# Optimization experiments

Measured on AMD Instinct MI355X. Metric: run time of the kernel, lower is better.

The kernel has to match this reference:

```python
import jax, jax.numpy as jnp
import numpy as np

N_NODES = 100000
N_EDGES = 3200000
D = 32


def _gat(x, edge_index, W, att_s, att_d, bias, heads, ch, neg_slope):
    """PyG-style GATConv (shared lin for src/dst, add_self_loops=False).
    x: [N, D_in], edge_index: [2, E], W: [heads*ch, D_in],
    att_s/att_d: [heads, ch], bias: [heads*ch]. Returns [N, heads*ch]."""
    n = x.shape[0]
    h = (x @ W.T).reshape(n, heads, ch)                      # [N,H,C]
    a_s = (h * att_s[None]).sum(-1)                           # [N,H]
    a_d = (h * att_d[None]).sum(-1)                           # [N,H]
    src, dst = edge_index[0], edge_index[1]
    logits = jax.nn.leaky_relu(a_s[src] + a_d[dst], neg_slope)  # [E,H]
    # segment softmax over edges grouped by destination node
    m = jax.ops.segment_max(logits, dst, num_segments=n)     # [N,H]
    m = jnp.where(jnp.isfinite(m), m, 0.0)                    # nodes w/ no in-edges
    ex = jnp.exp(logits - m[dst])                             # [E,H]
    denom = jax.ops.segment_sum(ex, dst, num_segments=n)     # [N,H]
    alpha = ex / (denom[dst] + 1e-16)                         # [E,H]
    out = jax.ops.segment_sum(alpha[:, :, None] * h[src], dst, num_segments=n)  # [N,H,C]
    return out.reshape(n, heads * ch) + bias


def setup_inputs() -> dict:
    key = jax.random.key(0)
    ks = jax.random.split(key, 16)
    x = jax.random.normal(ks[0], (N_NODES, D), dtype=jnp.float32)
    edge_index = jax.random.randint(ks[1], (2, N_EDGES), 0, N_NODES, dtype=jnp.int64)
    s = 1.0 / np.sqrt(D)
    return {
        "x": x,
        "edge_index": edge_index,
        "W1": jax.random.normal(ks[2], (32, D), dtype=jnp.float32) * s,
        "att_s1": jax.random.normal(ks[3], (2, 16), dtype=jnp.float32) * 0.05,
        "att_d1": jax.random.normal(ks[4], (2, 16), dtype=jnp.float32) * 0.05,
        "b1": jnp.full((32,), 0.1, dtype=jnp.float32),
        "ea1": jnp.ones((1,), dtype=jnp.float32),  # edge_activator
        "W2": jax.random.normal(ks[5], (32, 32), dtype=jnp.float32) * s,
        "att_s2": jax.random.normal(ks[6], (2, 16), dtype=jnp.float32) * 0.05,
        "att_d2": jax.random.normal(ks[7], (2, 16), dtype=jnp.float32) * 0.05,
        "b2": jnp.full((32,), 0.1, dtype=jnp.float32),
        "W3": jax.random.normal(ks[8], (32, 32), dtype=jnp.float32) * s,
        "att_s3": jax.random.normal(ks[9], (1, 32), dtype=jnp.float32) * 0.05,
        "att_d3": jax.random.normal(ks[10], (1, 32), dtype=jnp.float32) * 0.05,
        "b3": jnp.full((32,), 0.1, dtype=jnp.float32),
    }


def reference(x, edge_index, W1, att_s1, att_d1, b1, ea1,
              W2, att_s2, att_d2, b2, W3, att_s3, att_d3, b3):
    # --- layer 1 (negative_slope=0.01) ---
    h = _gat(x, edge_index, W1, att_s1, att_d1, b1, heads=2, ch=16, neg_slope=0.01)
    scale = jnp.tanh(ea1)[0]
    scale = jnp.where(scale < 0.1, 1.0, scale)  # 'continue' branch skips the scaling
    h = h * scale
    h = h + 0.05 * jax.lax.stop_gradient(h)      # h + 0.05*h.detach()
    h = jax.nn.elu(h)                            # eval path (training=False)
    h = jnp.clip(h, -3.0, 3.0)
    # --- layer 2 (default negative_slope=0.2) ---
    h = _gat(h, edge_index, W2, att_s2, att_d2, b2, heads=2, ch=16, neg_slope=0.2)
    h = jax.nn.elu(h)
    h = jnp.clip(h, -3.0, 3.0)
    # --- layer 3: heads=1, concat=False ---
    out = _gat(h, edge_index, W3, att_s3, att_d3, b3, heads=1, ch=32, neg_slope=0.2)
    return out
```

## Files before the change

kernel.cpp:

```cpp
#include <hip/hip_runtime.h>
#include <hip/hip_bf16.h>
#include <hip/hip_fp16.h>


#define NPB  128
#define CAPB 6144
#define PAD_SENTINEL 0xFFFFFFFFu

template <int H, int NL>
__device__ __forceinline__ void transform_body(
    const float* __restrict__ in, const float* __restrict__ W,
    const float* __restrict__ att_s, const float* __restrict__ att_d,
    __half* __restrict__ h16, float* __restrict__ a_s, float* __restrict__ a_d,
    int node0, int nlim, float (*Wl)[33], float (*xs)[32]) {
    constexpr int C = 32 / H;
    constexpr int NTH = NL * 32;
    int t = threadIdx.x;
    for (int i = t; i < 1024; i += NTH) Wl[i >> 5][i & 31] = W[i];
    int nl = t >> 5, o = t & 31;
    int node = node0 + nl;
    xs[nl][o] = (node < nlim) ? in[(size_t)node * 32 + o] : 0.f;
    __syncthreads();
    float acc = 0.f;
#pragma unroll
    for (int k = 0; k < 32; k++) acc = fmaf(xs[nl][k], Wl[o][k], acc);
    if (node < nlim) {
        h16[(size_t)node * 32 + o] = __float2half_rn(acc);
        float vs = acc * att_s[o];
        float vd = acc * att_d[o];
#pragma unroll
        for (int m = C / 2; m >= 1; m >>= 1) {
            vs += __shfl_xor(vs, m, 64);
            vd += __shfl_xor(vd, m, 64);
        }
        if ((o % C) == 0) {
            int hh = o / C;
            a_s[node * H + hh] = vs;
            a_d[node * H + hh] = vd;
        }
    }
}

__global__ void __launch_bounds__(1024)
k_bin_t1(const int* __restrict__ src, const int* __restrict__ dst,
         int* __restrict__ bucket_cursor, unsigned int* __restrict__ pairs,
         int e, int nb, int nbb,
         const float* __restrict__ in, const float* __restrict__ W,
         const float* __restrict__ att_s, const float* __restrict__ att_d,
         __half* __restrict__ h16, float* __restrict__ a_s,
         float* __restrict__ a_d, int nsplit) {
    __shared__ union {
        struct { int h[1024]; int bs[1024]; int cb[1024]; unsigned int stage[8192]; } b;
        struct { float Wl[32][33]; float xs[32][32]; } t;
    } sh;
    int t = threadIdx.x;
    if ((int)blockIdx.x >= nbb) {
        int node0 = ((int)blockIdx.x - nbb) * 32;
        transform_body<2, 32>(in, W, att_s, att_d, h16, a_s, a_d,
                              node0, nsplit, sh.t.Wl, sh.t.xs);
        return;
    }
    sh.b.h[t] = 0;
    __syncthreads();
    int e4 = e >> 2;
    int base4 = blockIdx.x * 2048;
    int boff[8];
    unsigned int pk[8];
#pragma unroll
    for (int k = 0; k < 2; k++) {
        int i4 = base4 + k * 1024 + t;
        if (i4 < e4) {
            int4 dv = ((const int4*)dst)[i4];
            int4 sv = ((const int4*)src)[i4];
            const int* dd = (const int*)&dv;
            const int* ss = (const int*)&sv;
#pragma unroll
            for (int j = 0; j < 4; j++) {
                int q = 4 * k + j;
                int d = dd[j];
                int b = d >> 7;
                pk[q] = ((unsigned int)ss[j] << 7) | (unsigned int)(d & 127);
                int off = atomicAdd(&sh.b.h[b], 1);
                boff[q] = (b << 16) | off;
            }
        } else {
#pragma unroll
            for (int j = 0; j < 4; j++) boff[4 * k + j] = -1;
        }
    }
    __syncthreads();
    if (t >= 128 && t - 128 < nb) {
        int b = t - 128;
        int c = sh.b.h[b];
        sh.b.cb[b] = c ? atomicAdd(&bucket_cursor[b], c) : 0;
    }
    if (t < 64) {
        int sum = 0;
#pragma unroll
        for (int j = 0; j < 16; j++) sum += sh.b.h[t * 16 + j];
        int run = sum;
#pragma unroll
        for (int off = 1; off < 64; off <<= 1) {
            int v = __shfl_up(run, off, 64);
            if (t >= off) run += v;
        }
        int base = run - sum;
#pragma unroll
        for (int j = 0; j < 16; j++) {
            int b = t * 16 + j;
            sh.b.bs[b] = base;
            base += sh.b.h[b];
        }
    }
    __syncthreads();
#pragma unroll
    for (int q = 0; q < 8; q++) {
        if (boff[q] >= 0) {
            int b = boff[q] >> 16;
            sh.b.stage[sh.b.bs[b] + (boff[q] & 0xFFFF)] = pk[q];
        }
    }
    __syncthreads();
    int wv = t >> 6, ln = t & 63;
    for (int b = wv; b < nb; b += 16) {
        int c = sh.b.h[b];
        if (c == 0) continue;
        int gb = sh.b.cb[b];
        int room = CAPB - gb;
        if (c > room) c = (room > 0) ? room : 0;
        unsigned int* dp = pairs + (size_t)b * CAPB + gb;
        const unsigned int* sp = sh.b.stage + sh.b.bs[b];
        for (int o = ln; o < c; o += 64) dp[o] = sp[o];
    }
    if (blockIdx.x == 0 && t < (e & 3)) {
        int i = (e & ~3) + t;
        int d = dst[i];
        int b = d >> 7;
        int r = atomicAdd(&bucket_cursor[b], 1);
        if (r < CAPB)
            pairs[(size_t)b * CAPB + r] =
                ((unsigned int)src[i] << 7) | (unsigned int)(d & 127);
    }
}

__global__ void __launch_bounds__(512)
k_sort_t1(const unsigned int* __restrict__ pairs,
          const int* __restrict__ bucket_cursor,
          int2* __restrict__ rowinfo, int* __restrict__ src_sorted,
          int n, int nb,
          const float* __restrict__ in, const float* __restrict__ W,
          const float* __restrict__ att_s, const float* __restrict__ att_d,
          __half* __restrict__ h16, float* __restrict__ a_s,
          float* __restrict__ a_d, int nsplit) {
    __shared__ union {
        struct { int cnt[NPB]; int cur[NPB]; int total;
                 unsigned int lp[CAPB]; int op[CAPB]; } s;
        struct { float Wl[32][33]; float xs[16][32]; } t;
    } sh;
    int t = threadIdx.x;
    if ((int)blockIdx.x >= nb) {
        int node0 = nsplit + ((int)blockIdx.x - nb) * 16;
        transform_body<2, 16>(in, W, att_s, att_d, h16, a_s, a_d,
                              node0, n, sh.t.Wl, sh.t.xs);
        return;
    }
    int b = blockIdx.x;
    int bbase = b * CAPB;
    int m = bucket_cursor[b];
    if (m > CAPB) m = CAPB;
    if (t < NPB) sh.s.cnt[t] = 0;
    __syncthreads();
    for (int cb = 0; cb < m; cb += 4096) {
        unsigned int pv[8];
#pragma unroll
        for (int u = 0; u < 8; u++) {
            int i = cb + u * 512 + t;
            pv[u] = (i < m) ? pairs[bbase + i] : PAD_SENTINEL;
        }
#pragma unroll
        for (int u = 0; u < 8; u++) {
            int i = cb + u * 512 + t;
            if (i < m) sh.s.lp[i] = pv[u];
            if (pv[u] != PAD_SENTINEL) atomicAdd(&sh.s.cnt[pv[u] & 127], 1);
        }
    }
    __syncthreads();
    if (t < 64) {
        int c0 = sh.s.cnt[2 * t];
        int c1 = sh.s.cnt[2 * t + 1];
        int sum = c0 + c1;
        int run = sum;
#pragma unroll
        for (int off = 1; off < 64; off <<= 1) {
            int v = __shfl_up(run, off, 64);
            if (t >= off) run += v;
        }
        int ex = run - sum;
        sh.s.cur[2 * t] = ex;
        sh.s.cur[2 * t + 1] = ex + c0;
        int node = b * NPB + 2 * t;
        if (node < n) rowinfo[node] = make_int2(bbase + ex, c0);
        if (node + 1 < n) rowinfo[node + 1] = make_int2(bbase + ex + c0, c1);
        if (t == 63) sh.s.total = run;
    }
    __syncthreads();
    for (int cb = 0; cb < m; cb += 4096) {
        unsigned int pv[8];
        int of[8];
#pragma unroll
        for (int u = 0; u < 8; u++) {
            int i = cb + u * 512 + t;
            pv[u] = (i < m) ? sh.s.lp[i] : PAD_SENTINEL;
        }
#pragma unroll
        for (int u = 0; u < 8; u++)
            if (pv[u] != PAD_SENTINEL) of[u] = atomicAdd(&sh.s.cur[pv[u] & 127], 1);
#pragma unroll
        for (int u = 0; u < 8; u++)
            if (pv[u] != PAD_SENTINEL) sh.s.op[of[u]] = (int)(pv[u] >> 7);
    }
    __syncthreads();
    int nt4 = (sh.s.total + 3) >> 2;
    int4* dst4 = (int4*)(src_sorted + bbase);
    const int4* src4 = (const int4*)sh.s.op;
    for (int i = t; i < nt4; i += 512) dst4[i] = src4[i];
}

template <int H, int EPI, int H2>
__global__ void __launch_bounds__(256)
k_edge_f(const int2* __restrict__ rowinfo, const int* __restrict__ src_sorted,
         const __half* __restrict__ h16,
         const float* __restrict__ a_s, const float* __restrict__ a_d,
         const float* __restrict__ bias, const float* __restrict__ ea,
         const float* __restrict__ Wn, const float* __restrict__ att_sn,
         const float* __restrict__ att_dn,
         __half* __restrict__ h16n, float* __restrict__ a_sn,
         float* __restrict__ a_dn, int n, float slope) {
    constexpr int CAP = 96;
    constexpr int RSTR = 2 * CAP + 16;
    __shared__ int lds_raw[8][H][RSTR];
    __shared__ float Wl2[32][33];
    __shared__ float row[8][32];
    int t = threadIdx.x;
    for (int i = t; i < 1024; i += 256) Wl2[i >> 5][i & 31] = Wn[i];
    __syncthreads();
    int nw = t >> 5;
    int hl = t & 31;
    int node = blockIdx.x * 8 + nw;
    if (node >= n) return;
    float ats = att_sn[hl], atd = att_dn[hl];
    int2 bi = rowinfo[node];
    int beg = bi.x, deg = bi.y;
    int padB = (deg + 15) & ~15;

    float ad[H];
#pragma unroll
    for (int hh = 0; hh < H; hh++) ad[hh] = a_d[node * H + hh];

    float ds[H];
#pragma unroll
    for (int hh = 0; hh < H; hh++) ds[hh] = 0.f;
    bool fast = (padB <= CAP);
    if (fast) {
        for (int idx = hl; idx < padB; idx += 32) {
            if (idx < deg) {
                int s = src_sorted[beg + idx];
                if (H == 2) {
                    float2 as2 = *(const float2*)((const char*)a_s + (unsigned)(s << 3));
                    float l0 = as2.x + ad[0]; l0 = fmaxf(l0, l0 * slope);
                    float l1 = as2.y + ad[1]; l1 = fmaxf(l1, l1 * slope);
                    float e0 = __expf(l0), e1 = __expf(l1);
                    ds[0] += e0; ds[1] += e1;
                    ((int2*)lds_raw[nw][0])[idx] = make_int2(s, __float_as_int(e0));
                    ((int2*)lds_raw[nw][H - 1])[idx] = make_int2(s, __float_as_int(e1));
                } else {
                    float l0 = a_s[s] + ad[0]; l0 = fmaxf(l0, l0 * slope);
                    float e0 = __expf(l0);
                    ds[0] += e0;
                    ((int2*)lds_raw[nw][0])[idx] = make_int2(s, __float_as_int(e0));
                }
            } else {
#pragma unroll
                for (int hh = 0; hh < H; hh++)
                    ((int2*)lds_raw[nw][hh])[idx] = make_int2(0, 0);
            }
        }
    } else {
        for (int idx = hl; idx < deg; idx += 32) {
            int s = src_sorted[beg + idx];
            if (H == 2) {
                float2 as2 = *(const float2*)((const char*)a_s + (unsigned)(s << 3));
                float l0 = as2.x + ad[0]; l0 = fmaxf(l0, l0 * slope);
                float l1 = as2.y + ad[1]; l1 = fmaxf(l1, l1 * slope);
                ds[0] += __expf(l0); ds[1] += __expf(l1);
            } else {
                float l0 = a_s[s] + ad[0]; l0 = fmaxf(l0, l0 * slope);
                ds[0] += __expf(l0);
            }
        }
    }

    int e2 = hl >> 4;
    int l16 = hl & 15;
    int hd = (H == 2) ? (l16 >> 3) : 0;
    int co = l16 << 2;
    float adh = ad[hd];
    float acc0 = 0.f, acc1 = 0.f;
    const char* hbase = (const char*)h16;
    const int* lb = &lds_raw[nw][hd][e2 * 4];

    if (fast) {
        for (int base = 0; base < padB; base += 16) {
            int4 qa = *(const int4*)(lb + base * 2);
            int4 qb = *(const int4*)(lb + base * 2 + 8);
            int4 qc = *(const int4*)(lb + base * 2 + 16);
            int4 qd = *(const int4*)(lb + base * 2 + 24);
            __half2 h0 = *(const __half2*)(hbase + (unsigned)((qa.x << 6) + co));
            __half2 h1 = *(const __half2*)(hbase + (unsigned)((qa.z << 6) + co));
            __half2 h2 = *(const __half2*)(hbase + (unsigned)((qb.x << 6) + co));
            __half2 h3 = *(const __half2*)(hbase + (unsigned)((qb.z << 6) + co));
            __half2 h4 = *(const __half2*)(hbase + (unsigned)((qc.x << 6) + co));
            __half2 h5 = *(const __half2*)(hbase + (unsigned)((qc.z << 6) + co));
            __half2 h6 = *(const __half2*)(hbase + (unsigned)((qd.x << 6) + co));
            __half2 h7 = *(const __half2*)(hbase + (unsigned)((qd.z << 6) + co));
            float xa0 = __int_as_float(qa.y), xa1 = __int_as_float(qa.w);
            float xb0 = __int_as_float(qb.y), xb1 = __int_as_float(qb.w);
            float xc0 = __int_as_float(qc.y), xc1 = __int_as_float(qc.w);
            float xd0 = __int_as_float(qd.y), xd1 = __int_as_float(qd.w);
            acc0 = fmaf(xa0, __half2float(__low2half(h0)), acc0);
            acc1 = fmaf(xa0, __half2float(__high2half(h0)), acc1);
            acc0 = fmaf(xa1, __half2float(__low2half(h1)), acc0);
            acc1 = fmaf(xa1, __half2float(__high2half(h1)), acc1);
            acc0 = fmaf(xb0, __half2float(__low2half(h2)), acc0);
            acc1 = fmaf(xb0, __half2float(__high2half(h2)), acc1);
            acc0 = fmaf(xb1, __half2float(__low2half(h3)), acc0);
            acc1 = fmaf(xb1, __half2float(__high2half(h3)), acc1);
            acc0 = fmaf(xc0, __half2float(__low2half(h4)), acc0);
            acc1 = fmaf(xc0, __half2float(__high2half(h4)), acc1);
            acc0 = fmaf(xc1, __half2float(__low2half(h5)), acc0);
            acc1 = fmaf(xc1, __half2float(__high2half(h5)), acc1);
            acc0 = fmaf(xd0, __half2float(__low2half(h6)), acc0);
            acc1 = fmaf(xd0, __half2float(__high2half(h6)), acc1);
            acc0 = fmaf(xd1, __half2float(__low2half(h7)), acc0);
            acc1 = fmaf(xd1, __half2float(__high2half(h7)), acc1);
        }
    } else {
        for (int base = 0; base < deg; base += 16) {
#pragma unroll
            for (int u = 0; u < 8; u++) {
                int idx = base + u * 2 + e2;
                int s = 0;
                float ex = 0.f;
                if (idx < deg) {
                    s = src_sorted[beg + idx];
                    float l = a_s[s * H + hd] + adh;
                    l = fmaxf(l, l * slope);
                    ex = __expf(l);
                }
                __half2 hv = *(const __half2*)(hbase + (unsigned)((s << 6) + co));
                acc0 = fmaf(ex, __half2float(__low2half(hv)), acc0);
                acc1 = fmaf(ex, __half2float(__high2half(hv)), acc1);
            }
        }
    }

#pragma unroll
    for (int hh = 0; hh < H; hh++) {
        float v = ds[hh];
#pragma unroll
        for (int m = 16; m >= 1; m >>= 1) v += __shfl_xor(v, m, 64);
        ds[hh] = 1.f / (v + 1e-16f);
    }
    acc0 += __shfl_xor(acc0, 16, 64);
    acc1 += __shfl_xor(acc1, 16, 64);

    float invd = ds[hd];
    float2 bv = *(const float2*)(bias + l16 * 2);
    float v0 = fmaf(acc0, invd, bv.x);
    float v1 = fmaf(acc1, invd, bv.y);
    if (EPI == 1) {
        float s0 = tanhf(ea[0]);
        if (s0 < 0.1f) s0 = 1.0f;
        s0 *= 1.05f;
        v0 *= s0; v1 *= s0;
    }
    v0 = (v0 > 0.f) ? v0 : expm1f(v0);
    v1 = (v1 > 0.f) ? v1 : expm1f(v1);
    v0 = fminf(3.f, fmaxf(-3.f, v0));
    v1 = fminf(3.f, fmaxf(-3.f, v1));

    if (hl < 16) {
        row[nw][2 * l16] = v0;
        row[nw][2 * l16 + 1] = v1;
    }
    float acc = 0.f;
#pragma unroll
    for (int k = 0; k < 32; k++) acc = fmaf(row[nw][k], Wl2[hl][k], acc);
    h16n[(size_t)node * 32 + hl] = __float2half_rn(acc);
    float vs = acc * ats;
    float vd = acc * atd;
    constexpr int C2 = 32 / H2;
#pragma unroll
    for (int m = C2 / 2; m >= 1; m >>= 1) {
        vs += __shfl_xor(vs, m, 64);
        vd += __shfl_xor(vd, m, 64);
    }
    if ((hl % C2) == 0) {
        int hh = hl / C2;
        a_sn[node * H2 + hh] = vs;
        a_dn[node * H2 + hh] = vd;
    }
}

template <int H, int EPI>
__global__ void k_edge(const int2* __restrict__ rowinfo, const int* __restrict__ src_sorted,
                       const __half* __restrict__ h16,
                       const float* __restrict__ a_s, const float* __restrict__ a_d,
                       const float* __restrict__ bias, const float* __restrict__ ea,
                       float* __restrict__ out, int n, float slope) {
    constexpr int CAP = 96;
    constexpr int RSTR = 2 * CAP + 16;
    __shared__ int lds_raw[8][H][RSTR];
    int nw = threadIdx.x >> 5;
    int hl = threadIdx.x & 31;
    int node = blockIdx.x * 8 + nw;
    if (node >= n) return;
    int2 bi = rowinfo[node];
    int beg = bi.x, deg = bi.y;
    int padB = (deg + 15) & ~15;

    float ad[H];
#pragma unroll
    for (int hh = 0; hh < H; hh++) ad[hh] = a_d[node * H + hh];

    float ds[H];
#pragma unroll
    for (int hh = 0; hh < H; hh++) ds[hh] = 0.f;
    bool fast = (padB <= CAP);
    if (fast) {
        for (int idx = hl; idx < padB; idx += 32) {
            if (idx < deg) {
                int s = src_sorted[beg + idx];
                if (H == 2) {
                    float2 as2 = *(const float2*)((const char*)a_s + (unsigned)(s << 3));
                    float l0 = as2.x + ad[0]; l0 = fmaxf(l0, l0 * slope);
                    float l1 = as2.y + ad[1]; l1 = fmaxf(l1, l1 * slope);
                    float e0 = __expf(l0), e1 = __expf(l1);
                    ds[0] += e0; ds[1] += e1;
                    ((int2*)lds_raw[nw][0])[idx] = make_int2(s, __float_as_int(e0));
                    ((int2*)lds_raw[nw][H - 1])[idx] = make_int2(s, __float_as_int(e1));
                } else {
                    float l0 = a_s[s] + ad[0]; l0 = fmaxf(l0, l0 * slope);
                    float e0 = __expf(l0);
                    ds[0] += e0;
                    ((int2*)lds_raw[nw][0])[idx] = make_int2(s, __float_as_int(e0));
                }
            } else {
#pragma unroll
                for (int hh = 0; hh < H; hh++)
                    ((int2*)lds_raw[nw][hh])[idx] = make_int2(0, 0);
            }
        }
    } else {
        for (int idx = hl; idx < deg; idx += 32) {
            int s = src_sorted[beg + idx];
            if (H == 2) {
                float2 as2 = *(const float2*)((const char*)a_s + (unsigned)(s << 3));
                float l0 = as2.x + ad[0]; l0 = fmaxf(l0, l0 * slope);
                float l1 = as2.y + ad[1]; l1 = fmaxf(l1, l1 * slope);
                ds[0] += __expf(l0); ds[1] += __expf(l1);
            } else {
                float l0 = a_s[s] + ad[0]; l0 = fmaxf(l0, l0 * slope);
                ds[0] += __expf(l0);
            }
        }
    }

    int e2 = hl >> 4;
    int l16 = hl & 15;
    int hd = (H == 2) ? (l16 >> 3) : 0;
    int co = l16 << 2;
    float adh = ad[hd];
    float acc0 = 0.f, acc1 = 0.f;
    const char* hbase = (const char*)h16;
    const int* lb = &lds_raw[nw][hd][e2 * 4];

    if (fast) {
        for (int base = 0; base < padB; base += 16) {
            int4 qa = *(const int4*)(lb + base * 2);
            int4 qb = *(const int4*)(lb + base * 2 + 8);
            int4 qc = *(const int4*)(lb + base * 2 + 16);
            int4 qd = *(const int4*)(lb + base * 2 + 24);
            __half2 h0 = *(const __half2*)(hbase + (unsigned)((qa.x << 6) + co));
            __half2 h1 = *(const __half2*)(hbase + (unsigned)((qa.z << 6) + co));
            __half2 h2 = *(const __half2*)(hbase + (unsigned)((qb.x << 6) + co));
            __half2 h3 = *(const __half2*)(hbase + (unsigned)((qb.z << 6) + co));
            __half2 h4 = *(const __half2*)(hbase + (unsigned)((qc.x << 6) + co));
            __half2 h5 = *(const __half2*)(hbase + (unsigned)((qc.z << 6) + co));
            __half2 h6 = *(const __half2*)(hbase + (unsigned)((qd.x << 6) + co));
            __half2 h7 = *(const __half2*)(hbase + (unsigned)((qd.z << 6) + co));
            float xa0 = __int_as_float(qa.y), xa1 = __int_as_float(qa.w);
            float xb0 = __int_as_float(qb.y), xb1 = __int_as_float(qb.w);
            float xc0 = __int_as_float(qc.y), xc1 = __int_as_float(qc.w);
            float xd0 = __int_as_float(qd.y), xd1 = __int_as_float(qd.w);
            acc0 = fmaf(xa0, __half2float(__low2half(h0)), acc0);
            acc1 = fmaf(xa0, __half2float(__high2half(h0)), acc1);
            acc0 = fmaf(xa1, __half2float(__low2half(h1)), acc0);
            acc1 = fmaf(xa1, __half2float(__high2half(h1)), acc1);
            acc0 = fmaf(xb0, __half2float(__low2half(h2)), acc0);
            acc1 = fmaf(xb0, __half2float(__high2half(h2)), acc1);
            acc0 = fmaf(xb1, __half2float(__low2half(h3)), acc0);
            acc1 = fmaf(xb1, __half2float(__high2half(h3)), acc1);
            acc0 = fmaf(xc0, __half2float(__low2half(h4)), acc0);
            acc1 = fmaf(xc0, __half2float(__high2half(h4)), acc1);
            acc0 = fmaf(xc1, __half2float(__low2half(h5)), acc0);
            acc1 = fmaf(xc1, __half2float(__high2half(h5)), acc1);
            acc0 = fmaf(xd0, __half2float(__low2half(h6)), acc0);
            acc1 = fmaf(xd0, __half2float(__high2half(h6)), acc1);
            acc0 = fmaf(xd1, __half2float(__low2half(h7)), acc0);
            acc1 = fmaf(xd1, __half2float(__high2half(h7)), acc1);
        }
    } else {
        for (int base = 0; base < deg; base += 16) {
#pragma unroll
            for (int u = 0; u < 8; u++) {
                int idx = base + u * 2 + e2;
                int s = 0;
                float ex = 0.f;
                if (idx < deg) {
                    s = src_sorted[beg + idx];
                    float l = a_s[s * H + hd] + adh;
                    l = fmaxf(l, l * slope);
                    ex = __expf(l);
                }
                __half2 hv = *(const __half2*)(hbase + (unsigned)((s << 6) + co));
                acc0 = fmaf(ex, __half2float(__low2half(hv)), acc0);
                acc1 = fmaf(ex, __half2float(__high2half(hv)), acc1);
            }
        }
    }

#pragma unroll
    for (int hh = 0; hh < H; hh++) {
        float v = ds[hh];
#pragma unroll
        for (int m = 16; m >= 1; m >>= 1) v += __shfl_xor(v, m, 64);
        ds[hh] = 1.f / (v + 1e-16f);
    }
    acc0 += __shfl_xor(acc0, 16, 64);
    acc1 += __shfl_xor(acc1, 16, 64);

    if (l16 == hl) {
        float invd = ds[hd];
        float2 bv = *(const float2*)(bias + l16 * 2);
        float v0 = fmaf(acc0, invd, bv.x);
        float v1 = fmaf(acc1, invd, bv.y);
        if (EPI == 1) {
            float s0 = tanhf(ea[0]);
            if (s0 < 0.1f) s0 = 1.0f;
            s0 *= 1.05f;
            v0 *= s0; v1 *= s0;
            v0 = (v0 > 0.f) ? v0 : expm1f(v0);
            v1 = (v1 > 0.f) ? v1 : expm1f(v1);
            v0 = fminf(3.f, fmaxf(-3.f, v0));
            v1 = fminf(3.f, fmaxf(-3.f, v1));
        } else if (EPI == 2) {
            v0 = (v0 > 0.f) ? v0 : expm1f(v0);
            v1 = (v1 > 0.f) ? v1 : expm1f(v1);
            v0 = fminf(3.f, fmaxf(-3.f, v0));
            v1 = fminf(3.f, fmaxf(-3.f, v1));
        }
        *(float2*)(out + (size_t)node * 32 + l16 * 2) = make_float2(v0, v1);
    }
}

extern "C" void kernel_launch(void* const* d_in, const int* in_sizes, int n_in,
                              void* d_out, int out_size, void* d_ws, size_t ws_size,
                              hipStream_t stream) {
    const float* x   = (const float*)d_in[0];
    const int*   ei  = (const int*)d_in[1];
    const float* W1  = (const float*)d_in[2];
    const float* as1 = (const float*)d_in[3];
    const float* ad1 = (const float*)d_in[4];
    const float* b1  = (const float*)d_in[5];
    const float* ea1 = (const float*)d_in[6];
    const float* W2  = (const float*)d_in[7];
    const float* as2 = (const float*)d_in[8];
    const float* ad2 = (const float*)d_in[9];
    const float* b2  = (const float*)d_in[10];
    const float* W3  = (const float*)d_in[11];
    const float* as3 = (const float*)d_in[12];
    const float* ad3 = (const float*)d_in[13];
    const float* b3  = (const float*)d_in[14];
    float* out = (float*)d_out;

    const int n = in_sizes[0] / 32;
    const int e = in_sizes[1] / 2;
    const int* src = ei;
    const int* dst = ei + e;
    const int nb = (n + NPB - 1) / NPB;

    char* w = (char*)d_ws;
    auto alloc = [&](size_t bytes) -> void* {
        void* p = (void*)w;
        w += (bytes + 255) & ~(size_t)255;
        return p;
    };
    __half* h16a    = (__half*)alloc((size_t)n * 32 * 2);
    float* a_s1     = (float*)alloc((size_t)n * 2 * 4);
    float* a_d1     = (float*)alloc((size_t)n * 2 * 4);
    int2* rowinfo   = (int2*)alloc((size_t)n * 8);
    int* bucket_cur = (int*)alloc((size_t)(nb + 1) * 4);
    int* src_sorted = (int*)alloc((size_t)nb * CAPB * 4);
    unsigned int* pairs = (unsigned int*)alloc((size_t)nb * CAPB * 4);

    char* sc = (char*)pairs;
    auto carve = [&](size_t bytes) -> void* {
        void* p = (void*)sc;
        sc += (bytes + 255) & ~(size_t)255;
        return p;
    };
    __half* h16b = (__half*)carve((size_t)n * 32 * 2);
    float* a_s2  = (float*)carve((size_t)n * 2 * 4);
    float* a_d2  = (float*)carve((size_t)n * 2 * 4);
    float* a_s3  = (float*)carve((size_t)n * 4);
    float* a_d3  = (float*)carve((size_t)n * 4);

    int nsplit = n / 2;
    nsplit = (nsplit + 31) & ~31;
    if (nsplit > n) nsplit = n;
    const int t1a = (nsplit + 31) / 32;
    const int t1b = (n - nsplit + 15) / 16;
    int e4 = e >> 2;
    const int nbb = (e4 + 2047) / 2048;

    hipMemsetAsync(bucket_cur, 0, (size_t)nb * 4, stream);
    k_bin_t1<<<nbb + t1a, 1024, 0, stream>>>(src, dst, bucket_cur, pairs, e, nb, nbb,
                                             x, W1, as1, ad1, h16a, a_s1, a_d1, nsplit);
    k_sort_t1<<<nb + t1b, 512, 0, stream>>>(pairs, bucket_cur, rowinfo, src_sorted, n, nb,
                                            x, W1, as1, ad1, h16a, a_s1, a_d1, nsplit);

    const int egrid = (n + 7) / 8;

    k_edge_f<2, 1, 2><<<egrid, 256, 0, stream>>>(rowinfo, src_sorted, h16a, a_s1, a_d1,
                                                 b1, ea1, W2, as2, ad2,
                                                 h16b, a_s2, a_d2, n, 0.01f);
    k_edge_f<2, 2, 1><<<egrid, 256, 0, stream>>>(rowinfo, src_sorted, h16b, a_s2, a_d2,
                                                 b2, nullptr, W3, as3, ad3,
                                                 h16a, a_s3, a_d3, n, 0.2f);
    k_edge<1, 0><<<egrid, 256, 0, stream>>>(rowinfo, src_sorted, h16a, a_s3, a_d3,
                                            b3, nullptr, out, n, 0.2f);
}
```

Before: 308.9 us.

## Fuse layer-1 edge aggregation into the bucket sort kernel

The layer-1 edge softmax/aggregation plus the layer-2 node transform move into the per-bucket sort kernel, which now processes its 128 destination nodes directly after sorting. The separate k_edge_f launch for layer 1 is removed. The layer-1 feature transform now runs entirely in the binning kernel instead of being split with the sort kernel. The intent is to save a launch and re-reading rowinfo/src_sorted, at the cost of fewer, heavier blocks (one per 128 nodes) with more LDS, and layer-1 transform work concentrated in one kernel.

```diff
diff --git a/kernel.cpp b/kernel.cpp
--- a/kernel.cpp
+++ b/kernel.cpp
@@ -5,6 +5,8 @@
 
 #define NPB  128
 #define CAPB 6144
+#define CAP  96
+#define RSTR 208
 #define PAD_SENTINEL 0xFFFFFFFFu
 
 template <int H, int NL>
@@ -48,7 +50,7 @@
          const float* __restrict__ in, const float* __restrict__ W,
          const float* __restrict__ att_s, const float* __restrict__ att_d,
          __half* __restrict__ h16, float* __restrict__ a_s,
-         float* __restrict__ a_d, int nsplit) {
+         float* __restrict__ a_d, int n) {
     __shared__ union {
         struct { int h[1024]; int bs[1024]; int cb[1024]; unsigned int stage[8192]; } b;
         struct { float Wl[32][33]; float xs[32][32]; } t;
@@ -57,7 +59,7 @@
     if ((int)blockIdx.x >= nbb) {
         int node0 = ((int)blockIdx.x - nbb) * 32;
         transform_body<2, 32>(in, W, att_s, att_d, h16, a_s, a_d,
-                              node0, nsplit, sh.t.Wl, sh.t.xs);
+                              node0, n, sh.t.Wl, sh.t.xs);
         return;
     }
     sh.b.h[t] = 0;
@@ -144,31 +146,35 @@
 }
 
 __global__ void __launch_bounds__(512)
-k_sort_t1(const unsigned int* __restrict__ pairs,
+k_sort_e1(const unsigned int* __restrict__ pairs,
           const int* __restrict__ bucket_cursor,
           int2* __restrict__ rowinfo, int* __restrict__ src_sorted,
           int n, int nb,
-          const float* __restrict__ in, const float* __restrict__ W,
-          const float* __restrict__ att_s, const float* __restrict__ att_d,
-          __half* __restrict__ h16, float* __restrict__ a_s,
-          float* __restrict__ a_d, int nsplit) {
-    __shared__ union {
-        struct { int cnt[NPB]; int cur[NPB]; int total;
-                 unsigned int lp[CAPB]; int op[CAPB]; } s;
-        struct { float Wl[32][33]; float xs[16][32]; } t;
-    } sh;
+          const __half* __restrict__ h16, const float* __restrict__ a_s,
+          const float* __restrict__ a_d,
+          const float* __restrict__ bias, const float* __restrict__ ea,
+          const float* __restrict__ Wn, const float* __restrict__ att_sn,
+          const float* __restrict__ att_dn,
+          __half* __restrict__ h16n, float* __restrict__ a_sn,
+          float* __restrict__ a_dn, float slope) {
+    __shared__ int cnt[NPB];
+    __shared__ int st[NPB];
+    __shared__ int cur[NPB];
+    __shared__ int total;
+    __shared__ __align__(16) union {
+        unsigned int lp[CAPB];
+        struct { float Wl2[32][33]; float row[16][32]; } e;
+    } ra;
+    __shared__ __align__(16) union {
+        int op[CAPB];
+        int stash[16][2][RSTR];
+    } rb;
+    int b = blockIdx.x;
     int t = threadIdx.x;
-    if ((int)blockIdx.x >= nb) {
-        int node0 = nsplit + ((int)blockIdx.x - nb) * 16;
-        transform_body<2, 16>(in, W, att_s, att_d, h16, a_s, a_d,
-                              node0, n, sh.t.Wl, sh.t.xs);
-        return;
-    }
-    int b = blockIdx.x;
     int bbase = b * CAPB;
     int m = bucket_cursor[b];
     if (m > CAPB) m = CAPB;
-    if (t < NPB) sh.s.cnt[t] = 0;
+    if (t < NPB) cnt[t] = 0;
     __syncthreads();
     for (int cb = 0; cb < m; cb += 4096) {
         unsigned int pv[8];
@@ -180,14 +186,14 @@
 #pragma unroll
         for (int u = 0; u < 8; u++) {
             int i = cb + u * 512 + t;
-            if (i < m) sh.s.lp[i] = pv[u];
-            if (pv[u] != PAD_SENTINEL) atomicAdd(&sh.s.cnt[pv[u] & 127], 1);
+            if (i < m) ra.lp[i] = pv[u];
+            if (pv[u] != PAD_SENTINEL) atomicAdd(&cnt[pv[u] & 127], 1);
         }
     }
     __syncthreads();
     if (t < 64) {
-        int c0 = sh.s.cnt[2 * t];
-        int c1 = sh.s.cnt[2 * t + 1];
+        int c0 = cnt[2 * t];
+        int c1 = cnt[2 * t + 1];
         int sum = c0 + c1;
         int run = sum;
 #pragma unroll
@@ -196,12 +202,14 @@
             if (t >= off) run += v;
         }
         int ex = run - sum;
-        sh.s.cur[2 * t] = ex;
-        sh.s.cur[2 * t + 1] = ex + c0;
+        st[2 * t] = ex;
+        st[2 * t + 1] = ex + c0;
+        cur[2 * t] = ex;
+        cur[2 * t + 1] = ex + c0;
         int node = b * NPB + 2 * t;
         if (node < n) rowinfo[node] = make_int2(bbase + ex, c0);
         if (node + 1 < n) rowinfo[node + 1] = make_int2(bbase + ex + c0, c1);
-        if (t == 63) sh.s.total = run;
+        if (t == 63) total = run;
     }
     __syncthreads();
     for (int cb = 0; cb < m; cb += 4096) {
@@ -210,20 +218,169 @@
 #pragma unroll
         for (int u = 0; u < 8; u++) {
             int i = cb + u * 512 + t;
-            pv[u] = (i < m) ? sh.s.lp[i] : PAD_SENTINEL;
+            pv[u] = (i < m) ? ra.lp[i] : PAD_SENTINEL;
         }
 #pragma unroll
         for (int u = 0; u < 8; u++)
-            if (pv[u] != PAD_SENTINEL) of[u] = atomicAdd(&sh.s.cur[pv[u] & 127], 1);
+            if (pv[u] != PAD_SENTINEL) of[u] = atomicAdd(&cur[pv[u] & 127], 1);
 #pragma unroll
         for (int u = 0; u < 8; u++)
-            if (pv[u] != PAD_SENTINEL) sh.s.op[of[u]] = (int)(pv[u] >> 7);
-    }
-    __syncthreads();
-    int nt4 = (sh.s.total + 3) >> 2;
-    int4* dst4 = (int4*)(src_sorted + bbase);
-    const int4* src4 = (const int4*)sh.s.op;
-    for (int i = t; i < nt4; i += 512) dst4[i] = src4[i];
+            if (pv[u] != PAD_SENTINEL) rb.op[of[u]] = (int)(pv[u] >> 7);
+    }
+    __syncthreads();
+    {
+        int nt4 = (total + 3) >> 2;
+        int4* dst4 = (int4*)(src_sorted + bbase);
+        const int4* src4 = (const int4*)rb.op;
+        for (int i = t; i < nt4; i += 512) dst4[i] = src4[i];
+        for (int i = t; i < 1024; i += 512) ra.e.Wl2[i >> 5][i & 31] = Wn[i];
+    }
+    __syncthreads();
+
+    int slot = t >> 5;
+    int hl = t & 31;
+    float ats = att_sn[hl], atd = att_dn[hl];
+    const char* hbase = (const char*)h16;
+    for (int j = slot; j < NPB; j += 16) {
+        int node = b * NPB + j;
+        if (node >= n) break;
+        int deg = cnt[j];
+        int beg = bbase + st[j];
+        int padB = (deg + 15) & ~15;
+        float ad0 = a_d[node * 2], ad1 = a_d[node * 2 + 1];
+        float ds0 = 0.f, ds1 = 0.f;
+        bool fastp = (padB <= CAP);
+        int* s0p = &rb.stash[slot][0][0];
+        int* s1p = &rb.stash[slot][1][0];
+        if (fastp) {
+            for (int idx = hl; idx < padB; idx += 32) {
+                if (idx < deg) {
+                    int s = src_sorted[beg + idx];
+                    float2 as2 = *(const float2*)((const char*)a_s + (unsigned)(s << 3));
+                    float l0 = as2.x + ad0; l0 = fmaxf(l0, l0 * slope);
+                    float l1 = as2.y + ad1; l1 = fmaxf(l1, l1 * slope);
+                    float e0 = __expf(l0), e1 = __expf(l1);
+                    ds0 += e0; ds1 += e1;
+                    ((int2*)s0p)[idx] = make_int2(s, __float_as_int(e0));
+                    ((int2*)s1p)[idx] = make_int2(s, __float_as_int(e1));
+                } else {
+                    ((int2*)s0p)[idx] = make_int2(0, 0);
+                    ((int2*)s1p)[idx] = make_int2(0, 0);
+                }
+            }
+        } else {
+            for (int idx = hl; idx < deg; idx += 32) {
+                int s = src_sorted[beg + idx];
+                float2 as2 = *(const float2*)((const char*)a_s + (unsigned)(s << 3));
+                float l0 = as2.x + ad0; l0 = fmaxf(l0, l0 * slope);
+                float l1 = as2.y + ad1; l1 = fmaxf(l1, l1 * slope);
+                ds0 += __expf(l0); ds1 += __expf(l1);
+            }
+        }
+        int e2 = hl >> 4;
+        int l16 = hl & 15;
+        int hd = l16 >> 3;
+        int co = l16 << 2;
+        float adh = hd ? ad1 : ad0;
+        float acc0 = 0.f, acc1 = 0.f;
+        const int* lb = &rb.stash[slot][hd][e2 * 4];
+        if (fastp) {
+            for (int base = 0; base < padB; base += 16) {
+                int4 qa = *(const int4*)(lb + base * 2);
+                int4 qb = *(const int4*)(lb + base * 2 + 8);
+                int4 qc = *(const int4*)(lb + base * 2 + 16);
+                int4 qd = *(const int4*)(lb + base * 2 + 24);
+                __half2 h0 = *(const __half2*)(hbase + (unsigned)((qa.x << 6) + co));
+                __half2 h1 = *(const __half2*)(hbase + (unsigned)((qa.z << 6) + co));
+                __half2 h2 = *(const __half2*)(hbase + (unsigned)((qb.x << 6) + co));
+                __half2 h3 = *(const __half2*)(hbase + (unsigned)((qb.z << 6) + co));
+                __half2 h4 = *(const __half2*)(hbase + (unsigned)((qc.x << 6) + co));
+                __half2 h5 = *(const __half2*)(hbase + (unsigned)((qc.z << 6) + co));
+                __half2 h6 = *(const __half2*)(hbase + (unsigned)((qd.x << 6) + co));
+                __half2 h7 = *(const __half2*)(hbase + (unsigned)((qd.z << 6) + co));
+                float xa0 = __int_as_float(qa.y), xa1 = __int_as_float(qa.w);
+                float xb0 = __int_as_float(qb.y), xb1 = __int_as_float(qb.w);
+                float xc0 = __int_as_float(qc.y), xc1 = __int_as_float(qc.w);
+                float xd0 = __int_as_float(qd.y), xd1 = __int_as_float(qd.w);
+                acc0 = fmaf(xa0, __half2float(__low2half(h0)), acc0);
+                acc1 = fmaf(xa0, __half2float(__high2half(h0)), acc1);
+                acc0 = fmaf(xa1, __half2float(__low2half(h1)), acc0);
+                acc1 = fmaf(xa1, __half2float(__high2half(h1)), acc1);
+                acc0 = fmaf(xb0, __half2float(__low2half(h2)), acc0);
+                acc1 = fmaf(xb0, __half2float(__high2half(h2)), acc1);
+                acc0 = fmaf(xb1, __half2float(__low2half(h3)), acc0);
+                acc1 = fmaf(xb1, __half2float(__high2half(h3)), acc1);
+                acc0 = fmaf(xc0, __half2float(__low2half(h4)), acc0);
+                acc1 = fmaf(xc0, __half2float(__high2half(h4)), acc1);
+                acc0 = fmaf(xc1, __half2float(__low2half(h5)), acc0);
+                acc1 = fmaf(xc1, __half2float(__high2half(h5)), acc1);
+                acc0 = fmaf(xd0, __half2float(__low2half(h6)), acc0);
+                acc1 = fmaf(xd0, __half2float(__high2half(h6)), acc1);
+                acc0 = fmaf(xd1, __half2float(__low2half(h7)), acc0);
+                acc1 = fmaf(xd1, __half2float(__high2half(h7)), acc1);
+            }
+        } else {
+            for (int base = 0; base < deg; base += 16) {
+#pragma unroll
+                for (int u = 0; u < 8; u++) {
+                    int idx = base + u * 2 + e2;
+                    int s = 0;
+                    float ex = 0.f;
+                    if (idx < deg) {
+                        s = src_sorted[beg + idx];
+                        float l = a_s[s * 2 + hd] + adh;
+                        l = fmaxf(l, l * slope);
+                        ex = __expf(l);
+                    }
+                    __half2 hv = *(const __half2*)(hbase + (unsigned)((s << 6) + co));
+                    acc0 = fmaf(ex, __half2float(__low2half(hv)), acc0);
+                    acc1 = fmaf(ex, __half2float(__high2half(hv)), acc1);
+                }
+            }
+        }
+#pragma unroll
+        for (int mm = 16; mm >= 1; mm >>= 1) {
+            ds0 += __shfl_xor(ds0, mm, 64);
+            ds1 += __shfl_xor(ds1, mm, 64);
+        }
+        acc0 += __shfl_xor(acc0, 16, 64);
+        acc1 += __shfl_xor(acc1, 16, 64);
+
+        float invd = 1.f / ((hd ? ds1 : ds0) + 1e-16f);
+        float2 bv = *(const float2*)(bias + l16 * 2);
+        float v0 = fmaf(acc0, invd, bv.x);
+        float v1 = fmaf(acc1, invd, bv.y);
+        float sc = tanhf(ea[0]);
+        if (sc < 0.1f) sc = 1.0f;
+        sc *= 1.05f;
+        v0 *= sc; v1 *= sc;
+        v0 = (v0 > 0.f) ? v0 : expm1f(v0);
+        v1 = (v1 > 0.f) ? v1 : expm1f(v1);
+        v0 = fminf(3.f, fmaxf(-3.f, v0));
+        v1 = fminf(3.f, fmaxf(-3.f, v1));
+
+        float* rowp = ra.e.row[slot];
+        if (hl < 16) {
+            rowp[2 * l16] = v0;
+            rowp[2 * l16 + 1] = v1;
+        }
+        float acc = 0.f;
+#pragma unroll
+        for (int k = 0; k < 32; k++) acc = fmaf(rowp[k], ra.e.Wl2[hl][k], acc);
+        h16n[(size_t)node * 32 + hl] = __float2half_rn(acc);
+        float vs = acc * ats;
+        float vd = acc * atd;
+#pragma unroll
+        for (int mm = 8; mm >= 1; mm >>= 1) {
+            vs += __shfl_xor(vs, mm, 64);
+            vd += __shfl_xor(vd, mm, 64);
+        }
+        if ((hl & 15) == 0) {
+            int hh = hl >> 4;
+            a_sn[node * 2 + hh] = vs;
+            a_dn[node * 2 + hh] = vd;
+        }
+    }
 }
 
 template <int H, int EPI, int H2>
@@ -236,8 +393,6 @@
          const float* __restrict__ att_dn,
          __half* __restrict__ h16n, float* __restrict__ a_sn,
          float* __restrict__ a_dn, int n, float slope) {
-    constexpr int CAP = 96;
-    constexpr int RSTR = 2 * CAP + 16;
     __shared__ int lds_raw[8][H][RSTR];
     __shared__ float Wl2[32][33];
     __shared__ float row[8][32];
@@ -418,8 +573,6 @@
                        const float* __restrict__ a_s, const float* __restrict__ a_d,
                        const float* __restrict__ bias, const float* __restrict__ ea,
                        float* __restrict__ out, int n, float slope) {
-    constexpr int CAP = 96;
-    constexpr int RSTR = 2 * CAP + 16;
     __shared__ int lds_raw[8][H][RSTR];
     int nw = threadIdx.x >> 5;
     int hl = threadIdx.x & 31;
@@ -555,16 +708,7 @@
         float2 bv = *(const float2*)(bias + l16 * 2);
         float v0 = fmaf(acc0, invd, bv.x);
         float v1 = fmaf(acc1, invd, bv.y);
-        if (EPI == 1) {
-            float s0 = tanhf(ea[0]);
-            if (s0 < 0.1f) s0 = 1.0f;
-            s0 *= 1.05f;
-            v0 *= s0; v1 *= s0;
-            v0 = (v0 > 0.f) ? v0 : expm1f(v0);
-            v1 = (v1 > 0.f) ? v1 : expm1f(v1);
-            v0 = fminf(3.f, fmaxf(-3.f, v0));
-            v1 = fminf(3.f, fmaxf(-3.f, v1));
-        } else if (EPI == 2) {
+        if (EPI == 2) {
             v0 = (v0 > 0.f) ? v0 : expm1f(v0);
             v1 = (v1 > 0.f) ? v1 : expm1f(v1);
             v0 = fminf(3.f, fmaxf(-3.f, v0));
@@ -607,8 +751,11 @@
         return p;
     };
     __half* h16a    = (__half*)alloc((size_t)n * 32 * 2);
+    __half* h16b    = (__half*)alloc((size_t)n * 32 * 2);
     float* a_s1     = (float*)alloc((size_t)n * 2 * 4);
     float* a_d1     = (float*)alloc((size_t)n * 2 * 4);
+    float* a_s2     = (float*)alloc((size_t)n * 2 * 4);
+    float* a_d2     = (float*)alloc((size_t)n * 2 * 4);
     int2* rowinfo   = (int2*)alloc((size_t)n * 8);
     int* bucket_cur = (int*)alloc((size_t)(nb + 1) * 4);
     int* src_sorted = (int*)alloc((size_t)nb * CAPB * 4);
@@ -620,31 +767,21 @@
         sc += (bytes + 255) & ~(size_t)255;
         return p;
     };
-    __half* h16b = (__half*)carve((size_t)n * 32 * 2);
-    float* a_s2  = (float*)carve((size_t)n * 2 * 4);
-    float* a_d2  = (float*)carve((size_t)n * 2 * 4);
-    float* a_s3  = (float*)carve((size_t)n * 4);
-    float* a_d3  = (float*)carve((size_t)n * 4);
-
-    int nsplit = n / 2;
-    nsplit = (nsplit + 31) & ~31;
-    if (nsplit > n) nsplit = n;
-    const int t1a = (nsplit + 31) / 32;
-    const int t1b = (n - nsplit + 15) / 16;
+    float* a_s3 = (float*)carve((size_t)n * 4);
+    float* a_d3 = (float*)carve((size_t)n * 4);
+
     int e4 = e >> 2;
     const int nbb = (e4 + 2047) / 2048;
+    const int t1a = (n + 31) / 32;
 
     hipMemsetAsync(bucket_cur, 0, (size_t)nb * 4, stream);
     k_bin_t1<<<nbb + t1a, 1024, 0, stream>>>(src, dst, bucket_cur, pairs, e, nb, nbb,
-                                             x, W1, as1, ad1, h16a, a_s1, a_d1, nsplit);
-    k_sort_t1<<<nb + t1b, 512, 0, stream>>>(pairs, bucket_cur, rowinfo, src_sorted, n, nb,
-                                            x, W1, as1, ad1, h16a, a_s1, a_d1, nsplit);
+                                             x, W1, as1, ad1, h16a, a_s1, a_d1, n);
+    k_sort_e1<<<nb, 512, 0, stream>>>(pairs, bucket_cur, rowinfo, src_sorted, n, nb,
+                                      h16a, a_s1, a_d1, b1, ea1,
+                                      W2, as2, ad2, h16b, a_s2, a_d2, 0.01f);
 
     const int egrid = (n + 7) / 8;
-
-    k_edge_f<2, 1, 2><<<egrid, 256, 0, stream>>>(rowinfo, src_sorted, h16a, a_s1, a_d1,
-                                                 b1, ea1, W2, as2, ad2,
-                                                 h16b, a_s2, a_d2, n, 0.01f);
     k_edge_f<2, 2, 1><<<egrid, 256, 0, stream>>>(rowinfo, src_sorted, h16b, a_s2, a_d2,
                                                  b2, nullptr, W3, as3, ad3,
                                                  h16a, a_s3, a_d3, n, 0.2f);
```

After: 323.0 us. +4.5%, slower.
